# Performance work log

Measured on AMD Instinct MI355X. Metric: run time of the kernel, lower is better.

## Reference

```python
import jax, jax.numpy as jnp
import numpy as np

N_ATOMS = 100000
N_EDGES = 1600000
N_FRAGS = 10000
N_FRAG_EDGES = 80000
D = 128


def setup_inputs() -> dict:
    key = jax.random.key(0)
    ks = jax.random.split(key, 16)
    s = 1.0 / np.sqrt(D)
    return {
        "x_atoms": jax.random.normal(ks[0], (N_ATOMS, D), jnp.float32),
        "edge_index": jax.random.randint(ks[1], (2, N_EDGES), 0, N_ATOMS),
        "edge_attr": jax.random.normal(ks[2], (N_EDGES, D), jnp.float32),
        "frag_index": jax.random.randint(ks[3], (2, N_FRAG_EDGES), 0, N_FRAGS),
        "x_frags": jax.random.normal(ks[4], (N_FRAGS, D), jnp.float32),
        "atom_to_frag_ids": jax.random.randint(ks[5], (N_ATOMS,), 0, N_FRAGS),
        # parameters (stored [in, out]); only layers actually used in forward
        "atom_w": jax.random.uniform(ks[6], (D, D), jnp.float32, -s, s),
        "atom_b": jax.random.uniform(ks[7], (D,), jnp.float32, -s, s),
        "edge_w": jax.random.uniform(ks[8], (D, D), jnp.float32, -s, s),
        "edge_b": jax.random.uniform(ks[9], (D,), jnp.float32, -s, s),
        "frag_w1": jax.random.uniform(ks[10], (D, 2 * D), jnp.float32, -s, s),
        "frag_b1": jax.random.uniform(ks[11], (2 * D,), jnp.float32, -s, s),
        "frag_w2": jax.random.uniform(ks[12], (2 * D, D), jnp.float32, -(1.0 / np.sqrt(2 * D)), 1.0 / np.sqrt(2 * D)),
        "frag_b2": jax.random.uniform(ks[13], (D,), jnp.float32, -(1.0 / np.sqrt(2 * D)), 1.0 / np.sqrt(2 * D)),
    }


def reference(x_atoms, edge_index, edge_attr, frag_index, x_frags,
              atom_to_frag_ids, atom_w, atom_b, edge_w, edge_b,
              frag_w1, frag_b1, frag_w2, frag_b2):
    n = x_atoms.shape[0]
    n_frags = x_frags.shape[0]

    # add self loops
    loop = jnp.arange(n, dtype=edge_index.dtype)
    src = jnp.concatenate([edge_index[0], loop])
    tgt = jnp.concatenate([edge_index[1], loop])
    self_loop_attr = jnp.zeros((n, edge_attr.shape[1]), edge_attr.dtype)
    edge_attr_full = jnp.concatenate([edge_attr, self_loop_attr], axis=0)

    # embeddings
    h = x_atoms @ atom_w + atom_b                      # [N, D]
    _e = edge_attr_full @ edge_w + edge_b              # computed but unused (as in source)

    # symmetric degree normalization over source-node degree
    deg = jax.ops.segment_sum(jnp.ones_like(src, dtype=h.dtype), src, num_segments=n)
    dinv = jnp.where(deg > 0, deg ** -0.5, 0.0)
    norm = dinv[src] * dinv[tgt]                       # [E+N]

    # gather - scale - scatter_add
    msg = h[src] * norm[:, None]                       # [E+N, D]
    x_atoms_new = jax.ops.segment_sum(msg, tgt, num_segments=n)

    # pool atoms into fragments
    frag_feats = jax.ops.segment_sum(x_atoms_new, atom_to_frag_ids, num_segments=n_frags)

    # fragment-level message passing
    fsrc, ftgt = frag_index[0], frag_index[1]
    frag_sum = jax.ops.segment_sum(frag_feats[fsrc], ftgt, num_segments=n_frags)

    # frag_mlp: Linear(D, 2D) -> ReLU -> Linear(2D, D)
    x_frags_new = jax.nn.relu(frag_sum @ frag_w1 + frag_b1) @ frag_w2 + frag_b2
    return (x_atoms_new, x_frags_new)
```

## Files before the change

kernel.cpp:

```cpp
#include <hip/hip_runtime.h>

constexpr int DD = 128;

typedef __attribute__((ext_vector_type(8))) short short8_t;
typedef __attribute__((ext_vector_type(8))) unsigned short ushort8_t;
typedef __attribute__((ext_vector_type(4))) float f32x4;

__device__ __forceinline__ float bf2f(unsigned short u) {
  union { unsigned int i; float f; } c;
  c.i = ((unsigned int)u) << 16;
  return c.f;
}
__device__ __forceinline__ unsigned short f2bf(float f) {
  union { float f; unsigned int i; } c;
  c.f = f;
  unsigned int x = c.i;
  x += 0x7fff + ((x >> 16) & 1);
  return (unsigned short)(x >> 16);
}

__global__ void __launch_bounds__(256) counts_k(
    const int* __restrict__ esrc, const int* __restrict__ etgt, int E,
    const int* __restrict__ a2f, int N, const int* __restrict__ ftgt, int FE,
    int* __restrict__ cnt_src, int* __restrict__ cnt_tgt,
    int* __restrict__ cnt_a2f, int* __restrict__ cnt_fe,
    int* __restrict__ rank_tgt, int* __restrict__ rank_a2f, int* __restrict__ rank_fe) {
  int i = blockIdx.x * 256 + threadIdx.x;
  if (i < E) {
    atomicAdd(&cnt_src[esrc[i]], 1);
    rank_tgt[i] = atomicAdd(&cnt_tgt[etgt[i]], 1);
  } else if (i < E + N) {
    int j = i - E;
    rank_a2f[j] = atomicAdd(&cnt_a2f[a2f[j]], 1);
  } else if (i < E + N + FE) {
    int e = i - E - N;
    rank_fe[e] = atomicAdd(&cnt_fe[ftgt[e]], 1);
  }
}

__global__ void __launch_bounds__(256) mfma_h_k(
    const float* __restrict__ x, const float* __restrict__ W,
    const float* __restrict__ bias, unsigned short* __restrict__ hout, int nrows) {
  __shared__ unsigned int wt[8192];

  const int tid = threadIdx.x;
  const int rbase = blockIdx.x * 128;

  {
    int c = tid & 127;
    int half = tid >> 7;
#pragma unroll 4
    for (int j = 0; j < 32; j++) {
      int p = j * 2 + half;
      int k = p * 2;
      float w0 = W[k * 128 + c];
      float w1 = W[(k + 1) * 128 + c];
      unsigned int packed = (unsigned int)f2bf(w0) | ((unsigned int)f2bf(w1) << 16);
      wt[(64 * c + p) ^ ((c & 7) << 2)] = packed;
    }
  }

  const int wave = tid >> 6;
  const int lane = tid & 63;
  const int l15 = lane & 15;
  const int kg = lane >> 4;

  float bcol[8];
#pragma unroll
  for (int ct = 0; ct < 8; ct++) bcol[ct] = bias[ct * 16 + l15];

  __syncthreads();

  f32x4 acc[2][8];
#pragma unroll
  for (int rt = 0; rt < 2; rt++)
#pragma unroll
    for (int ct = 0; ct < 8; ct++) acc[rt][ct] = (f32x4)(0.f);

#pragma unroll
  for (int ks = 0; ks < 4; ks++) {
    int kcol = ks * 32 + kg * 8;
    short8_t a[2];
#pragma unroll
    for (int rt = 0; rt < 2; rt++) {
      int row = rbase + wave * 32 + rt * 16 + l15;
      if (row < nrows) {
        const float4* xr = reinterpret_cast<const float4*>(x + (size_t)row * 128 + kcol);
        float4 v0 = xr[0], v1 = xr[1];
        a[rt][0] = (short)f2bf(v0.x); a[rt][1] = (short)f2bf(v0.y);
        a[rt][2] = (short)f2bf(v0.z); a[rt][3] = (short)f2bf(v0.w);
        a[rt][4] = (short)f2bf(v1.x); a[rt][5] = (short)f2bf(v1.y);
        a[rt][6] = (short)f2bf(v1.z); a[rt][7] = (short)f2bf(v1.w);
      } else {
#pragma unroll
        for (int e = 0; e < 8; e++) a[rt][e] = 0;
      }
    }
#pragma unroll
    for (int ct = 0; ct < 8; ct++) {
      int col = ct * 16 + l15;
      int dw0 = (64 * col + ks * 16 + kg * 4) ^ ((col & 7) << 2);
      short8_t b = *reinterpret_cast<const short8_t*>(&wt[dw0]);
      acc[0][ct] = __builtin_amdgcn_mfma_f32_16x16x32_bf16(a[0], b, acc[0][ct], 0, 0, 0);
      acc[1][ct] = __builtin_amdgcn_mfma_f32_16x16x32_bf16(a[1], b, acc[1][ct], 0, 0, 0);
    }
  }

#pragma unroll
  for (int rt = 0; rt < 2; rt++)
#pragma unroll
    for (int ct = 0; ct < 8; ct++)
#pragma unroll
      for (int i = 0; i < 4; i++) {
        int gr = rbase + wave * 32 + rt * 16 + kg * 4 + i;
        if (gr < nrows)
          hout[(size_t)gr * 128 + ct * 16 + l15] = f2bf(acc[rt][ct][i] + bcol[ct]);
      }
}

__global__ void __launch_bounds__(256) scanA_k(
    const int* __restrict__ cnt_tgt, int n, int nb, int* __restrict__ bsums,
    const int* __restrict__ cnt_a2f, int* __restrict__ off_a2f,
    const int* __restrict__ cnt_fe, int* __restrict__ off_fe, int nf) {
  __shared__ int s[256];
  int t = threadIdx.x;
  int bid = blockIdx.x;
  if (bid < nb) {
    int base = bid * 1024;
    int v = 0;
    for (int i = t; i < 1024; i += 256) {
      int g = base + i;
      if (g < n) v += cnt_tgt[g];
    }
    s[t] = v;
    __syncthreads();
    for (int d = 128; d > 0; d >>= 1) {
      if (t < d) s[t] += s[t + d];
      __syncthreads();
    }
    if (t == 0) bsums[bid] = s[0];
  } else {
    const int* in = (bid == nb) ? cnt_a2f : cnt_fe;
    int* off = (bid == nb) ? off_a2f : off_fe;
    int carry = 0;
    for (int base = 0; base < nf; base += 256) {
      int v = (base + t < nf) ? in[base + t] : 0;
      __syncthreads();
      s[t] = v;
      __syncthreads();
      for (int d = 1; d < 256; d <<= 1) {
        int u = (t >= d) ? s[t - d] : 0;
        __syncthreads();
        s[t] += u;
        __syncthreads();
      }
      if (base + t < nf) off[base + t] = s[t] - v + carry;
      carry += s[255];
    }
  }
}

__global__ void __launch_bounds__(256) scanB_k(
    const int* __restrict__ in, int n, const int* __restrict__ bsums,
    int* __restrict__ off, const int* __restrict__ cnt_src,
    float* __restrict__ dinv) {
  __shared__ int s[256];
  int t = threadIdx.x;
  int bid = blockIdx.x;
  s[t] = (t < bid) ? bsums[t] : 0;
  __syncthreads();
  for (int d = 128; d > 0; d >>= 1) {
    if (t < d) s[t] += s[t + d];
    __syncthreads();
  }
  int prefix = s[0];
  __syncthreads();

  int base = bid * 1024 + t * 4;
  int a0 = (base + 0 < n) ? in[base + 0] : 0;
  int a1 = (base + 1 < n) ? in[base + 1] : 0;
  int a2 = (base + 2 < n) ? in[base + 2] : 0;
  int a3 = (base + 3 < n) ? in[base + 3] : 0;
  int tot = a0 + a1 + a2 + a3;
  s[t] = tot;
  __syncthreads();
  for (int d = 1; d < 256; d <<= 1) {
    int u = (t >= d) ? s[t - d] : 0;
    __syncthreads();
    s[t] += u;
    __syncthreads();
  }
  int pre = s[t] - tot + prefix;
  int e0 = pre, e1 = pre + a0, e2 = e1 + a1, e3 = e2 + a2;
  if (base + 0 < n) { off[base + 0] = e0; dinv[base + 0] = rsqrtf((float)(cnt_src[base + 0] + 1)); }
  if (base + 1 < n) { off[base + 1] = e1; dinv[base + 1] = rsqrtf((float)(cnt_src[base + 1] + 1)); }
  if (base + 2 < n) { off[base + 2] = e2; dinv[base + 2] = rsqrtf((float)(cnt_src[base + 2] + 1)); }
  if (base + 3 < n) { off[base + 3] = e3; dinv[base + 3] = rsqrtf((float)(cnt_src[base + 3] + 1)); }
}

__global__ void __launch_bounds__(256) fill_scale_k(
    const int* __restrict__ esrc, const int* __restrict__ etgt, int E,
    const int* __restrict__ a2f, int N,
    const int* __restrict__ fsrc, const int* __restrict__ ftgt, int FE,
    const int* __restrict__ off_tgt, const int* __restrict__ rank_tgt,
    const int* __restrict__ off_a2f, const int* __restrict__ rank_a2f,
    const int* __restrict__ off_fe, const int* __restrict__ rank_fe,
    int* __restrict__ csr_src, int* __restrict__ aids, int* __restrict__ csr_fs,
    unsigned short* __restrict__ h, const float* __restrict__ dinv, int nbf) {
  if ((int)blockIdx.x >= nbf) {
    int idx = ((int)blockIdx.x - nbf) * 256 + threadIdx.x;
    if (idx < N * 16) {
      float d = dinv[idx >> 4];
      ushort8_t v = reinterpret_cast<ushort8_t*>(h)[idx];
#pragma unroll
      for (int e = 0; e < 8; e++) v[e] = f2bf(bf2f(v[e]) * d);
      reinterpret_cast<ushort8_t*>(h)[idx] = v;
    }
    return;
  }
  int i = blockIdx.x * 256 + threadIdx.x;
  if (i < E) {
    csr_src[off_tgt[etgt[i]] + rank_tgt[i]] = esrc[i];
  } else if (i < E + N) {
    int j = i - E;
    aids[off_a2f[a2f[j]] + rank_a2f[j]] = j;
  } else if (i < E + N + FE) {
    int e = i - E - N;
    csr_fs[off_fe[ftgt[e]] + rank_fe[e]] = fsrc[e];
  }
}

__global__ void __launch_bounds__(256) edge_gather_k(
    const int* __restrict__ off, const int* __restrict__ cnt,
    const int* __restrict__ csr_src, const unsigned short* __restrict__ h,
    const float* __restrict__ dinv, float* __restrict__ out, int n) {
  int tn = blockIdx.x * 16 + (threadIdx.x >> 4);
  if (tn >= n) return;
  int lane = threadIdx.x & 15;
  const ushort8_t* h8 = reinterpret_cast<const ushort8_t*>(h);
  ushort8_t hv = h8[(size_t)tn * 16 + lane];
  float acc[8];
#pragma unroll
  for (int e = 0; e < 8; e++) acc[e] = bf2f(hv[e]);
  int s0 = off[tn], c = cnt[tn];
  int i = 0;
  for (; i + 4 <= c; i += 4) {
    int s1 = csr_src[s0 + i + 0];
    int s2 = csr_src[s0 + i + 1];
    int s3 = csr_src[s0 + i + 2];
    int s4 = csr_src[s0 + i + 3];
    ushort8_t v1 = h8[(size_t)s1 * 16 + lane];
    ushort8_t v2 = h8[(size_t)s2 * 16 + lane];
    ushort8_t v3 = h8[(size_t)s3 * 16 + lane];
    ushort8_t v4 = h8[(size_t)s4 * 16 + lane];
#pragma unroll
    for (int e = 0; e < 8; e++)
      acc[e] += (bf2f(v1[e]) + bf2f(v2[e])) + (bf2f(v3[e]) + bf2f(v4[e]));
  }
  for (; i < c; i++) {
    int s1 = csr_src[s0 + i];
    ushort8_t v1 = h8[(size_t)s1 * 16 + lane];
#pragma unroll
    for (int e = 0; e < 8; e++) acc[e] += bf2f(v1[e]);
  }
  float dt = dinv[tn];
  float4* o4 = reinterpret_cast<float4*>(out) + (size_t)tn * 32 + lane * 2;
  o4[0] = make_float4(acc[0] * dt, acc[1] * dt, acc[2] * dt, acc[3] * dt);
  o4[1] = make_float4(acc[4] * dt, acc[5] * dt, acc[6] * dt, acc[7] * dt);
}

__global__ void __launch_bounds__(256) seg_gather_k(
    const int* __restrict__ off, const int* __restrict__ cnt,
    const int* __restrict__ ids, const float* __restrict__ src_rows,
    float* __restrict__ dst, int n) {
  int f = blockIdx.x * 8 + (threadIdx.x >> 5);
  if (f >= n) return;
  int lane = threadIdx.x & 31;
  const float4* s4 = reinterpret_cast<const float4*>(src_rows);
  float ax = 0.f, ay = 0.f, az = 0.f, aw = 0.f;
  int s0 = off[f], c = cnt[f];
  int i = 0;
  for (; i + 2 <= c; i += 2) {
    int a1 = ids[s0 + i], a2 = ids[s0 + i + 1];
    float4 v1 = s4[(size_t)a1 * 32 + lane];
    float4 v2 = s4[(size_t)a2 * 32 + lane];
    ax += v1.x + v2.x; ay += v1.y + v2.y; az += v1.z + v2.z; aw += v1.w + v2.w;
  }
  if (i < c) {
    int a1 = ids[s0 + i];
    float4 v1 = s4[(size_t)a1 * 32 + lane];
    ax += v1.x; ay += v1.y; az += v1.z; aw += v1.w;
  }
  reinterpret_cast<float4*>(dst)[(size_t)f * 32 + lane] = make_float4(ax, ay, az, aw);
}

__global__ void __launch_bounds__(256) mlp_k(
    const float* __restrict__ fs, const float* __restrict__ W1,
    const float* __restrict__ b1, const float* __restrict__ W2,
    const float* __restrict__ b2, float* __restrict__ out, int nrows) {
  __shared__ float xs[32 * 128];
  __shared__ float hs[32 * 256];
  const int tid = threadIdx.x;
  const int rbase = blockIdx.x * 32;

  const float4* in4 = reinterpret_cast<const float4*>(fs);
  for (int idx = tid; idx < 32 * 32; idx += 256) {
    int r = idx / 32, kk = idx % 32;
    int gr = rbase + r;
    float4 v = make_float4(0.f, 0.f, 0.f, 0.f);
    if (gr < nrows) v = in4[(size_t)gr * 32 + kk];
    reinterpret_cast<float4*>(xs)[idx] = v;
  }
  __syncthreads();

  {
    float acc[32];
    float b = b1[tid];
#pragma unroll
    for (int m = 0; m < 32; m++) acc[m] = b;
#pragma unroll 4
    for (int k = 0; k < 128; k++) {
      float w = W1[k * 256 + tid];
#pragma unroll
      for (int m = 0; m < 32; m++) acc[m] += xs[m * 128 + k] * w;
    }
#pragma unroll
    for (int m = 0; m < 32; m++) hs[m * 256 + tid] = fmaxf(acc[m], 0.f);
  }
  __syncthreads();

  {
    const int c2 = tid & 127;
    const int g = tid >> 7;
    float acc[16];
    float b = b2[c2];
#pragma unroll
    for (int m = 0; m < 16; m++) acc[m] = b;
#pragma unroll 4
    for (int k = 0; k < 256; k++) {
      float w = W2[k * 128 + c2];
#pragma unroll
      for (int m = 0; m < 16; m++) acc[m] += hs[(g + m * 2) * 256 + k] * w;
    }
#pragma unroll
    for (int m = 0; m < 16; m++) {
      int gr = rbase + g + m * 2;
      if (gr < nrows) out[(size_t)gr * 128 + c2] = acc[m];
    }
  }
}

extern "C" void kernel_launch(void* const* d_in, const int* in_sizes, int n_in,
                              void* d_out, int out_size, void* d_ws, size_t ws_size,
                              hipStream_t stream) {
  const float* x_atoms    = (const float*)d_in[0];
  const int*   edge_index = (const int*)d_in[1];
  const int*   frag_index = (const int*)d_in[3];
  const int*   a2f     = (const int*)d_in[5];
  const float* atom_w  = (const float*)d_in[6];
  const float* atom_b  = (const float*)d_in[7];
  const float* frag_w1 = (const float*)d_in[10];
  const float* frag_b1 = (const float*)d_in[11];
  const float* frag_w2 = (const float*)d_in[12];
  const float* frag_b2 = (const float*)d_in[13];

  const int N  = in_sizes[0] / DD;
  const int E  = in_sizes[1] / 2;
  const int FE = in_sizes[3] / 2;
  const int NF = in_sizes[4] / DD;

  const int* esrc = edge_index;
  const int* etgt = edge_index + E;
  const int* fsrc = frag_index;
  const int* ftgt = frag_index + FE;

  float* out_atoms = (float*)d_out;
  float* out_frags = out_atoms + (size_t)N * DD;

  char* ws = (char*)d_ws;
  size_t off_b = 0;
  auto alloc = [&](size_t bytes) {
    void* p = ws + off_b;
    off_b += (bytes + 255) & ~(size_t)255;
    return p;
  };
  unsigned short* h = (unsigned short*)alloc((size_t)N * DD * 2);
  float* dinv     = (float*)alloc((size_t)N * 4);
  int*   cnts     = (int*)alloc(((size_t)2 * N + 2 * NF) * 4);
  int*   cnt_src  = cnts;
  int*   cnt_tgt  = cnts + N;
  int*   cnt_a2f  = cnts + 2 * N;
  int*   cnt_fe   = cnts + 2 * N + NF;
  int*   off_tgt  = (int*)alloc((size_t)N * 4);
  int*   rank_tgt = (int*)alloc((size_t)E * 4);
  int*   csr_src  = (int*)alloc((size_t)E * 4);
  int*   off_a2f  = (int*)alloc((size_t)NF * 4);
  int*   rank_a2f = (int*)alloc((size_t)N * 4);
  int*   aids     = (int*)alloc((size_t)N * 4);
  int*   off_fe   = (int*)alloc((size_t)NF * 4);
  int*   rank_fe  = (int*)alloc((size_t)FE * 4);
  int*   csr_fs   = (int*)alloc((size_t)FE * 4);
  int*   bsums    = (int*)alloc(1024 * 4);
  float* ff       = (float*)alloc((size_t)NF * DD * 4);
  float* fs       = (float*)alloc((size_t)NF * DD * 4);

  hipMemsetAsync(cnts, 0, ((size_t)2 * N + 2 * NF) * 4, stream);

  int nb_cnt = (E + N + FE + 255) / 256;
  counts_k<<<nb_cnt, 256, 0, stream>>>(
      esrc, etgt, E, a2f, N, ftgt, FE,
      cnt_src, cnt_tgt, cnt_a2f, cnt_fe, rank_tgt, rank_a2f, rank_fe);

  mfma_h_k<<<(N + 127) / 128, 256, 0, stream>>>(x_atoms, atom_w, atom_b, h, N);

  int nb1 = (N + 1023) / 1024;
  scanA_k<<<nb1 + 2, 256, 0, stream>>>(cnt_tgt, N, nb1, bsums,
                                       cnt_a2f, off_a2f, cnt_fe, off_fe, NF);
  scanB_k<<<nb1, 256, 0, stream>>>(cnt_tgt, N, bsums, off_tgt, cnt_src, dinv);

  int nb_scale = (N * 16 + 255) / 256;
  fill_scale_k<<<nb_cnt + nb_scale, 256, 0, stream>>>(
      esrc, etgt, E, a2f, N, fsrc, ftgt, FE,
      off_tgt, rank_tgt, off_a2f, rank_a2f, off_fe, rank_fe,
      csr_src, aids, csr_fs, h, dinv, nb_cnt);

  edge_gather_k<<<(N + 15) / 16, 256, 0, stream>>>(off_tgt, cnt_tgt, csr_src, h, dinv, out_atoms, N);
  seg_gather_k<<<(NF + 7) / 8, 256, 0, stream>>>(off_a2f, cnt_a2f, aids, out_atoms, ff, NF);
  seg_gather_k<<<(NF + 7) / 8, 256, 0, stream>>>(off_fe, cnt_fe, csr_fs, ff, fs, NF);

  mlp_k<<<(NF + 31) / 32, 256, 0, stream>>>(fs, frag_w1, frag_b1, frag_w2, frag_b2, out_frags, NF);
}
```

Baseline: 426.7 us.

## Fuse dinv scaling into the MFMA epilogue and parallelize edge gather over a full wavefront

The GEMM that produces h now runs after the degree scan and multiplies each output row by dinv in its epilogue. This removes the separate read-modify-write pass over h that fill_scale_k used to do. The edge gather now gives one node a full 64-lane wave: four groups of 16 lanes split the neighbour list and combine their sums with xor shuffles. That raises memory-level parallelism per node, at the cost of more idle lanes on low-degree nodes.

```diff
diff --git a/kernel.cpp b/kernel.cpp
--- a/kernel.cpp
+++ b/kernel.cpp
@@ -40,7 +40,8 @@
 
 __global__ void __launch_bounds__(256) mfma_h_k(
     const float* __restrict__ x, const float* __restrict__ W,
-    const float* __restrict__ bias, unsigned short* __restrict__ hout, int nrows) {
+    const float* __restrict__ bias, const float* __restrict__ dinv,
+    unsigned short* __restrict__ hout, int nrows) {
   __shared__ unsigned int wt[8192];
 
   const int tid = threadIdx.x;
@@ -68,6 +69,14 @@
   float bcol[8];
 #pragma unroll
   for (int ct = 0; ct < 8; ct++) bcol[ct] = bias[ct * 16 + l15];
+  float dv[8];
+#pragma unroll
+  for (int rt = 0; rt < 2; rt++)
+#pragma unroll
+    for (int i = 0; i < 4; i++) {
+      int gr = rbase + wave * 32 + rt * 16 + kg * 4 + i;
+      dv[rt * 4 + i] = (gr < nrows) ? dinv[gr] : 0.f;
+    }
 
   __syncthreads();
 
@@ -114,7 +123,8 @@
       for (int i = 0; i < 4; i++) {
         int gr = rbase + wave * 32 + rt * 16 + kg * 4 + i;
         if (gr < nrows)
-          hout[(size_t)gr * 128 + ct * 16 + l15] = f2bf(acc[rt][ct][i] + bcol[ct]);
+          hout[(size_t)gr * 128 + ct * 16 + l15] =
+              f2bf((acc[rt][ct][i] + bcol[ct]) * dv[rt * 4 + i]);
       }
 }
 
@@ -198,26 +208,14 @@
   if (base + 3 < n) { off[base + 3] = e3; dinv[base + 3] = rsqrtf((float)(cnt_src[base + 3] + 1)); }
 }
 
-__global__ void __launch_bounds__(256) fill_scale_k(
+__global__ void __launch_bounds__(256) fill_k(
     const int* __restrict__ esrc, const int* __restrict__ etgt, int E,
     const int* __restrict__ a2f, int N,
     const int* __restrict__ fsrc, const int* __restrict__ ftgt, int FE,
     const int* __restrict__ off_tgt, const int* __restrict__ rank_tgt,
     const int* __restrict__ off_a2f, const int* __restrict__ rank_a2f,
     const int* __restrict__ off_fe, const int* __restrict__ rank_fe,
-    int* __restrict__ csr_src, int* __restrict__ aids, int* __restrict__ csr_fs,
-    unsigned short* __restrict__ h, const float* __restrict__ dinv, int nbf) {
-  if ((int)blockIdx.x >= nbf) {
-    int idx = ((int)blockIdx.x - nbf) * 256 + threadIdx.x;
-    if (idx < N * 16) {
-      float d = dinv[idx >> 4];
-      ushort8_t v = reinterpret_cast<ushort8_t*>(h)[idx];
-#pragma unroll
-      for (int e = 0; e < 8; e++) v[e] = f2bf(bf2f(v[e]) * d);
-      reinterpret_cast<ushort8_t*>(h)[idx] = v;
-    }
-    return;
-  }
+    int* __restrict__ csr_src, int* __restrict__ aids, int* __restrict__ csr_fs) {
   int i = blockIdx.x * 256 + threadIdx.x;
   if (i < E) {
     csr_src[off_tgt[etgt[i]] + rank_tgt[i]] = esrc[i];
@@ -234,39 +232,51 @@
     const int* __restrict__ off, const int* __restrict__ cnt,
     const int* __restrict__ csr_src, const unsigned short* __restrict__ h,
     const float* __restrict__ dinv, float* __restrict__ out, int n) {
-  int tn = blockIdx.x * 16 + (threadIdx.x >> 4);
+  int tn = blockIdx.x * 4 + (threadIdx.x >> 6);
   if (tn >= n) return;
-  int lane = threadIdx.x & 15;
+  int lane = threadIdx.x & 63;
+  int j = lane >> 4, l15 = lane & 15;
   const ushort8_t* h8 = reinterpret_cast<const ushort8_t*>(h);
-  ushort8_t hv = h8[(size_t)tn * 16 + lane];
+
   float acc[8];
-#pragma unroll
-  for (int e = 0; e < 8; e++) acc[e] = bf2f(hv[e]);
+  if (j == 0) {
+    ushort8_t hv = h8[(size_t)tn * 16 + l15];
+#pragma unroll
+    for (int e = 0; e < 8; e++) acc[e] = bf2f(hv[e]);
+  } else {
+#pragma unroll
+    for (int e = 0; e < 8; e++) acc[e] = 0.f;
+  }
+
   int s0 = off[tn], c = cnt[tn];
-  int i = 0;
-  for (; i + 4 <= c; i += 4) {
-    int s1 = csr_src[s0 + i + 0];
-    int s2 = csr_src[s0 + i + 1];
-    int s3 = csr_src[s0 + i + 2];
-    int s4 = csr_src[s0 + i + 3];
-    ushort8_t v1 = h8[(size_t)s1 * 16 + lane];
-    ushort8_t v2 = h8[(size_t)s2 * 16 + lane];
-    ushort8_t v3 = h8[(size_t)s3 * 16 + lane];
-    ushort8_t v4 = h8[(size_t)s4 * 16 + lane];
-#pragma unroll
-    for (int e = 0; e < 8; e++)
-      acc[e] += (bf2f(v1[e]) + bf2f(v2[e])) + (bf2f(v3[e]) + bf2f(v4[e]));
-  }
-  for (; i < c; i++) {
-    int s1 = csr_src[s0 + i];
-    ushort8_t v1 = h8[(size_t)s1 * 16 + lane];
-#pragma unroll
-    for (int e = 0; e < 8; e++) acc[e] += bf2f(v1[e]);
-  }
-  float dt = dinv[tn];
-  float4* o4 = reinterpret_cast<float4*>(out) + (size_t)tn * 32 + lane * 2;
-  o4[0] = make_float4(acc[0] * dt, acc[1] * dt, acc[2] * dt, acc[3] * dt);
-  o4[1] = make_float4(acc[4] * dt, acc[5] * dt, acc[6] * dt, acc[7] * dt);
+  int i = j;
+  for (; i + 4 < c; i += 8) {
+    int sa = csr_src[s0 + i];
+    int sb = csr_src[s0 + i + 4];
+    ushort8_t va = h8[(size_t)sa * 16 + l15];
+    ushort8_t vb = h8[(size_t)sb * 16 + l15];
+#pragma unroll
+    for (int e = 0; e < 8; e++) acc[e] += bf2f(va[e]) + bf2f(vb[e]);
+  }
+  if (i < c) {
+    int sa = csr_src[s0 + i];
+    ushort8_t va = h8[(size_t)sa * 16 + l15];
+#pragma unroll
+    for (int e = 0; e < 8; e++) acc[e] += bf2f(va[e]);
+  }
+
+#pragma unroll
+  for (int e = 0; e < 8; e++) {
+    acc[e] += __shfl_xor(acc[e], 16, 64);
+    acc[e] += __shfl_xor(acc[e], 32, 64);
+  }
+
+  if (j == 0) {
+    float dt = dinv[tn];
+    float4* o4 = reinterpret_cast<float4*>(out) + (size_t)tn * 32 + l15 * 2;
+    o4[0] = make_float4(acc[0] * dt, acc[1] * dt, acc[2] * dt, acc[3] * dt);
+    o4[1] = make_float4(acc[4] * dt, acc[5] * dt, acc[6] * dt, acc[7] * dt);
+  }
 }
 
 __global__ void __launch_bounds__(256) seg_gather_k(
@@ -411,20 +421,19 @@
       esrc, etgt, E, a2f, N, ftgt, FE,
       cnt_src, cnt_tgt, cnt_a2f, cnt_fe, rank_tgt, rank_a2f, rank_fe);
 
-  mfma_h_k<<<(N + 127) / 128, 256, 0, stream>>>(x_atoms, atom_w, atom_b, h, N);
-
   int nb1 = (N + 1023) / 1024;
   scanA_k<<<nb1 + 2, 256, 0, stream>>>(cnt_tgt, N, nb1, bsums,
                                        cnt_a2f, off_a2f, cnt_fe, off_fe, NF);
   scanB_k<<<nb1, 256, 0, stream>>>(cnt_tgt, N, bsums, off_tgt, cnt_src, dinv);
 
-  int nb_scale = (N * 16 + 255) / 256;
-  fill_scale_k<<<nb_cnt + nb_scale, 256, 0, stream>>>(
+  mfma_h_k<<<(N + 127) / 128, 256, 0, stream>>>(x_atoms, atom_w, atom_b, dinv, h, N);
+
+  fill_k<<<nb_cnt, 256, 0, stream>>>(
       esrc, etgt, E, a2f, N, fsrc, ftgt, FE,
       off_tgt, rank_tgt, off_a2f, rank_a2f, off_fe, rank_fe,
-      csr_src, aids, csr_fs, h, dinv, nb_cnt);
-
-  edge_gather_k<<<(N + 15) / 16, 256, 0, stream>>>(off_tgt, cnt_tgt, csr_src, h, dinv, out_atoms, N);
+      csr_src, aids, csr_fs);
+
+  edge_gather_k<<<(N + 3) / 4, 256, 0, stream>>>(off_tgt, cnt_tgt, csr_src, h, dinv, out_atoms, N);
   seg_gather_k<<<(NF + 7) / 8, 256, 0, stream>>>(off_a2f, cnt_a2f, aids, out_atoms, ff, NF);
   seg_gather_k<<<(NF + 7) / 8, 256, 0, stream>>>(off_fe, cnt_fe, csr_fs, ff, fs, NF);
 
```

Measured after the change: 427.3 us. About the same (+0.1%).
